# Performance work log

Hardware: AMD Instinct MI355X
Metric: run time of the kernel (lower is better)

## Reference

```python
import jax, jax.numpy as jnp
import numpy as np

N_NODES = 50000
N_FEAT = 128
N_EDGES = 800000
HEADS1 = 4
HID1 = 64
HID2 = 128
N_CLASSES = 10
N_GRAPHS = 512
NEG_SLOPE_ATT = 0.2   # GATConv attention leaky relu
NEG_SLOPE_ACT = 0.01  # F.leaky_relu default between layers


def setup_inputs() -> dict:
    key = jax.random.key(0)
    ks = jax.random.split(key, 20)
    s = 0.05
    inp = {
        'x': jax.random.normal(ks[0], (N_NODES, N_FEAT), dtype=jnp.float32),
        'edge_index': jax.random.randint(ks[1], (2, N_EDGES), 0, N_NODES, dtype=jnp.int64),
        'edge_attr': jax.random.normal(ks[2], (N_EDGES, 8), dtype=jnp.float32),
        'batch': jnp.sort(jax.random.randint(ks[3], (N_NODES,), 0, N_GRAPHS, dtype=jnp.int64)),
        # conv1: F -> HID1, heads=4, concat
        'W1': jax.random.normal(ks[4], (N_FEAT, HEADS1 * HID1), dtype=jnp.float32) * s,
        'a_src1': jax.random.normal(ks[5], (HEADS1, HID1), dtype=jnp.float32) * s,
        'a_dst1': jax.random.normal(ks[6], (HEADS1, HID1), dtype=jnp.float32) * s,
        'b1': jnp.zeros((HEADS1 * HID1,), dtype=jnp.float32),
        # conv2: 4*HID1 -> HID2, heads=1
        'W2': jax.random.normal(ks[7], (HEADS1 * HID1, HID2), dtype=jnp.float32) * s,
        'a_src2': jax.random.normal(ks[8], (1, HID2), dtype=jnp.float32) * s,
        'a_dst2': jax.random.normal(ks[9], (1, HID2), dtype=jnp.float32) * s,
        'b2': jnp.zeros((HID2,), dtype=jnp.float32),
        # conv3: HID2 -> N_CLASSES, heads=1
        'W3': jax.random.normal(ks[10], (HID2, N_CLASSES), dtype=jnp.float32) * s,
        'a_src3': jax.random.normal(ks[11], (1, N_CLASSES), dtype=jnp.float32) * s,
        'a_dst3': jax.random.normal(ks[12], (1, N_CLASSES), dtype=jnp.float32) * s,
        'b3': jnp.zeros((N_CLASSES,), dtype=jnp.float32),
    }
    return inp


def gat_conv(x, src, dst, W, a_src, a_dst, b, n_nodes, heads, ch):
    """PyG GATConv (concat=True, add_self_loops already applied in src/dst)."""
    h = (x @ W).reshape(n_nodes, heads, ch)            # [N,H,C]
    al_s = (h * a_src).sum(-1)                          # [N,H]
    al_d = (h * a_dst).sum(-1)                          # [N,H]
    e = jax.nn.leaky_relu(al_s[src] + al_d[dst], NEG_SLOPE_ATT)  # [E,H]
    # segment softmax over incoming edges per destination node
    m = jax.ops.segment_max(e, dst, num_segments=n_nodes)
    ex = jnp.exp(e - m[dst])
    den = jax.ops.segment_sum(ex, dst, num_segments=n_nodes)
    alpha = ex / (den[dst] + 1e-16)                     # [E,H]
    out = jax.ops.segment_sum(h[src] * alpha[..., None], dst, num_segments=n_nodes)
    return out.reshape(n_nodes, heads * ch) + b


def reference(x, edge_index, edge_attr, batch,
              W1, a_src1, a_dst1, b1,
              W2, a_src2, a_dst2, b2,
              W3, a_src3, a_dst3, b3):
    # GATConv adds self-loops by default; edge_attr unused (edge_dim=None)
    loops = jnp.arange(N_NODES, dtype=edge_index.dtype)
    src = jnp.concatenate([edge_index[0], loops])
    dst = jnp.concatenate([edge_index[1], loops])

    h = gat_conv(x, src, dst, W1, a_src1, a_dst1, b1, N_NODES, HEADS1, HID1)
    h = jax.nn.leaky_relu(h, NEG_SLOPE_ACT)
    h = gat_conv(h, src, dst, W2, a_src2, a_dst2, b2, N_NODES, 1, HID2)
    h = jax.nn.leaky_relu(h, NEG_SLOPE_ACT)
    h = gat_conv(h, src, dst, W3, a_src3, a_dst3, b3, N_NODES, 1, N_CLASSES)

    pooled = jax.ops.segment_sum(h, batch, num_segments=N_GRAPHS)  # global_add_pool
    return jax.nn.log_softmax(pooled, axis=1), pooled
```

## Files before the change

kernel.cpp:

```cpp
#include <hip/hip_runtime.h>
#include <math.h>

#define NNODES 50000
#define MPAD   50048
#define NFEAT  128
#define NEDGE  800000
#define ETOT   (NEDGE + NNODES)
#define H1     4
#define O1     256
#define C2     128
#define C3     10
#define NGRAPH 512

#define NBKT   196
#define NBLK1  831
#define EPB    1024
#define SCM    (NBKT * NBLK1)
#define SCB    637

typedef __attribute__((ext_vector_type(8))) short short8;
typedef __attribute__((ext_vector_type(4))) float f32x4;
typedef __attribute__((ext_vector_type(2))) float f32x2;

__device__ __forceinline__ unsigned short f2b(float f) {
  unsigned int u = __float_as_uint(f);
  u += 0x7fffu + ((u >> 16) & 1u);
  return (unsigned short)(u >> 16);
}
__device__ __forceinline__ float b2f(unsigned short u) {
  return __uint_as_float(((unsigned int)u) << 16);
}
__device__ __forceinline__ float readlane_f(float v, int l) {
  return __uint_as_float((unsigned)__builtin_amdgcn_readlane(__float_as_uint(v), l));
}


__global__ void k_prep(const float* __restrict__ W1, const float* __restrict__ as1,
                       const float* __restrict__ ad1,
                       float* __restrict__ was, float* __restrict__ wad) {
  int tid = threadIdx.x;
  int h = tid >> 7, k = tid & 127;
  float s = 0.f, d = 0.f;
  for (int j = 0; j < 64; ++j) {
    float w = W1[(size_t)k * 256 + h * 64 + j];
    s += w * as1[h * 64 + j];
    d += w * ad1[h * 64 + j];
  }
  was[h * 128 + k] = s;
  wad[h * 128 + k] = d;
}

#define NB_CVT 12500

__global__ __launch_bounds__(256) void k_front(
    const int* __restrict__ src_e, const int* __restrict__ dst_e,
    int* __restrict__ hists,
    const float* __restrict__ X, unsigned short* __restrict__ Xb,
    const float* __restrict__ W1,
    const float* __restrict__ was, const float* __restrict__ wad,
    float* __restrict__ als, float* __restrict__ ald,
    unsigned short* __restrict__ W1p,
    const float* __restrict__ W2, unsigned short* __restrict__ W2p,
    const float* __restrict__ W3, unsigned short* __restrict__ W3p) {
  const int b = blockIdx.x;
  const int tid = threadIdx.x;
  if (b < NBLK1) {
    __shared__ int h[NBKT];
    if (tid < NBKT) h[tid] = 0;
    __syncthreads();
    const int base = b * EPB;
#pragma unroll
    for (int r = 0; r < 4; ++r) {
      int e = base + r * 256 + tid;
      if (e < ETOT) {
        int d = (e < NEDGE) ? dst_e[e] : (e - NEDGE);
        atomicAdd(&h[d >> 8], 1);
      }
    }
    __syncthreads();
    if (tid < NBKT) hists[tid * NBLK1 + b] = h[tid];
  } else if (b < NBLK1 + NB_CVT) {
    const int n = (b - NBLK1) * 4 + (tid >> 6);
    const int lane = tid & 63;
    const int k0 = lane * 2;
    float2 xv = *(const float2*)(X + (size_t)n * 128 + k0);
    ushort2 o; o.x = f2b(xv.x); o.y = f2b(xv.y);
    *(ushort2*)(Xb + (size_t)n * 128 + k0) = o;
    float s[4], d[4];
#pragma unroll
    for (int h = 0; h < 4; ++h) {
      float2 wsv = *(const float2*)(was + h * 128 + k0);
      float2 wdv = *(const float2*)(wad + h * 128 + k0);
      s[h] = xv.x * wsv.x + xv.y * wsv.y;
      d[h] = xv.x * wdv.x + xv.y * wdv.y;
    }
#pragma unroll
    for (int m = 1; m < 64; m <<= 1)
#pragma unroll
      for (int h = 0; h < 4; ++h) { s[h] += __shfl_xor(s[h], m); d[h] += __shfl_xor(d[h], m); }
    if (lane == 0) {
#pragma unroll
      for (int h = 0; h < 4; ++h) {
        als[(size_t)n * 4 + h] = s[h];
        ald[(size_t)n * 4 + h] = d[h];
      }
    }
  } else if (b < NBLK1 + NB_CVT + 128) {
    int idx = (b - NBLK1 - NB_CVT) * 256 + tid;
    int h = idx >> 13, r = idx & 8191;
    int j = r & 7, lane = (r >> 3) & 63, t = r >> 9;
    int ks = t & 3, nt = t >> 2;
    int k = ks * 32 + (lane >> 4) * 8 + j;
    int n = nt * 16 + (lane & 15);
    W1p[idx] = f2b(W1[(size_t)k * 256 + h * 64 + n]);
  } else if (b < NBLK1 + NB_CVT + 256) {
    int idx = (b - NBLK1 - NB_CVT - 128) * 256 + tid;
    int j = idx & 7, lane = (idx >> 3) & 63, t = idx >> 9;
    int ks = t % 8, nt = t / 8;
    int k = ks * 32 + (lane >> 4) * 8 + j;
    int n = nt * 16 + (lane & 15);
    W2p[idx] = f2b(W2[(size_t)k * C2 + n]);
  } else {
    int idx = (b - NBLK1 - NB_CVT - 256) * 256 + tid;
    int j = idx & 7, lane = (idx >> 3) & 63, t = idx >> 9;
    int ks = t & 3, nt = t >> 2;
    int k = ks * 32 + (lane >> 4) * 8 + j;
    int n = nt * 16 + (lane & 15);
    W3p[idx] = f2b((n < C3) ? W3[(size_t)k * C3 + n] : 0.f);
  }
}


__global__ __launch_bounds__(256) void k_scanA2(const int* __restrict__ a,
                                                int* __restrict__ bsum) {
  int idx = blockIdx.x * 256 + threadIdx.x;
  int v = (idx < SCM) ? a[idx] : 0;
#pragma unroll
  for (int m = 1; m < 64; m <<= 1) v += __shfl_xor(v, m);
  __shared__ int ws[4];
  int lane = threadIdx.x & 63, wid = threadIdx.x >> 6;
  if (lane == 0) ws[wid] = v;
  __syncthreads();
  if (threadIdx.x == 0) bsum[blockIdx.x] = ws[0] + ws[1] + ws[2] + ws[3];
}

__global__ __launch_bounds__(256) void k_scanMid(int* __restrict__ bsum) {
  __shared__ int ws[4];
  __shared__ int carry_s;
  const int tid = threadIdx.x, lane = tid & 63, wid = tid >> 6;
  if (tid == 0) carry_s = 0;
  __syncthreads();
  for (int base = 0; base < SCB; base += 256) {
    int j = base + tid;
    int v = (j < SCB) ? bsum[j] : 0;
    int s = v;
#pragma unroll
    for (int m = 1; m < 64; m <<= 1) {
      int t = __shfl_up(s, m);
      if (lane >= m) s += t;
    }
    if (lane == 63) ws[wid] = s;
    __syncthreads();
    int woff = 0;
#pragma unroll
    for (int k = 0; k < 4; ++k)
      if (k < wid) woff += ws[k];
    int c = carry_s;
    int tot = ws[0] + ws[1] + ws[2] + ws[3];
    if (j < SCB) bsum[j] = c + woff + s - v;
    __syncthreads();
    if (tid == 0) carry_s = c + tot;
    __syncthreads();
  }
}

__global__ __launch_bounds__(256) void k_scanB2(int* __restrict__ a,
                                                const int* __restrict__ bsum,
                                                int* __restrict__ cb) {
  const int b = blockIdx.x, tid = threadIdx.x;
  const int lane = tid & 63, wid = tid >> 6;
  __shared__ int ws[4];
  int idx = b * 256 + tid;
  int v = (idx < SCM) ? a[idx] : 0;
  int s = v;
#pragma unroll
  for (int m = 1; m < 64; m <<= 1) {
    int t = __shfl_up(s, m);
    if (lane >= m) s += t;
  }
  if (lane == 63) ws[wid] = s;
  __syncthreads();
  int woff = 0;
#pragma unroll
  for (int k = 0; k < 4; ++k)
    if (k < wid) woff += ws[k];
  int excl = bsum[b] + woff + s - v;
  if (idx < SCM) {
    a[idx] = excl;
    if (idx % NBLK1 == 0) cb[idx / NBLK1] = excl;
  }
  if (b == 0 && tid == 0) cb[NBKT] = ETOT;
}


__global__ __launch_bounds__(256) void k_part1(const int* __restrict__ src_e,
                                               const int* __restrict__ dst_e,
                                               const int* __restrict__ offs,
                                               unsigned* __restrict__ coarse) {
  __shared__ int cur[NBKT];
  const int b = blockIdx.x;
  const int tid = threadIdx.x;
  if (tid < NBKT) cur[tid] = offs[tid * NBLK1 + b];
  __syncthreads();
  const int base = b * EPB;
#pragma unroll
  for (int r = 0; r < 4; ++r) {
    int e = base + r * 256 + tid;
    if (e < ETOT) {
      int d, s;
      if (e < NEDGE) { d = dst_e[e]; s = src_e[e]; }
      else           { d = e - NEDGE; s = e - NEDGE; }
      int pos = atomicAdd(&cur[d >> 8], 1);
      coarse[pos] = ((unsigned)d << 16) | (unsigned)s;
    }
  }
}


__global__ __launch_bounds__(256) void k_bucket(const unsigned* __restrict__ coarse,
                                                const int* __restrict__ cb,
                                                int* __restrict__ rowptr,
                                                int* __restrict__ srcs) {
  const int b = blockIdx.x;
  const int tid = threadIdx.x;
  const int lane = tid & 63, wid = tid >> 6;
  const int lo = cb[b], hi = cb[b + 1];
  __shared__ int h[256];
  __shared__ int cur[256];
  __shared__ int ws[4];
  h[tid] = 0;
  __syncthreads();
  for (int i = lo + tid; i < hi; i += 256)
    atomicAdd(&h[(coarse[i] >> 16) & 255], 1);
  __syncthreads();
  int v = h[tid];
  int s = v;
#pragma unroll
  for (int m = 1; m < 64; m <<= 1) {
    int t = __shfl_up(s, m);
    if (lane >= m) s += t;
  }
  if (lane == 63) ws[wid] = s;
  __syncthreads();
  int woff = 0;
#pragma unroll
  for (int k = 0; k < 4; ++k)
    if (k < wid) woff += ws[k];
  int ex = woff + s - v;
  cur[tid] = lo + ex;
  int d = b * 256 + tid;
  if (d < NNODES) rowptr[d] = lo + ex;
  if (b == NBKT - 1 && tid == 0) rowptr[NNODES] = ETOT;
  __syncthreads();
  for (int i = lo + tid; i < hi; i += 256) {
    unsigned c = coarse[i];
    int pos = atomicAdd(&cur[(c >> 16) & 255], 1);
    srcs[pos] = (int)(c & 0xffffu);
  }
}


__global__ __launch_bounds__(512) void k_aggP(const int* __restrict__ rowptr,
                                              const int* __restrict__ srcs,
                                              const unsigned short* __restrict__ Xb,
                                              const float* __restrict__ als,
                                              const float* __restrict__ ald,
                                              const unsigned short* __restrict__ W1p,
                                              const float* __restrict__ b1,
                                              unsigned short* __restrict__ act1) {
  __shared__ float exs[8][16][4];
  __shared__ unsigned short Pl[8][4][128];
  const int wv = threadIdx.x >> 6;
  const int n = blockIdx.x * 8 + wv;
  const int lane = threadIdx.x & 63;
  const int r0 = rowptr[n], r1 = rowptr[n + 1];
  const int e_lane = lane & 15, hh = lane >> 4;
  const float aldv = ald[(size_t)n * 4 + hh];
  const int ch0 = lane * 2;
  f32x2 ah0 = {0.f, 0.f}, ah1 = {0.f, 0.f}, ah2 = {0.f, 0.f}, ah3 = {0.f, 0.f};
  float den = 0.f;
  for (int i0 = r0; i0 < r1; i0 += 16) {
    const int take = r1 - i0;
    int sidx = srcs[min(i0 + e_lane, r1 - 1)];
    float ev = als[(size_t)sidx * 4 + hh] + aldv;
    ev = (ev > 0.f) ? ev : 0.2f * ev;
    float exv = (e_lane < take) ? __expf(ev) : 0.f;
    den += exv;
    exs[wv][e_lane][hh] = exv;
    unsigned hv[16];
#pragma unroll
    for (int m = 0; m < 16; ++m) {
      int s = __builtin_amdgcn_readlane(sidx, m);
      hv[m] = *(const unsigned*)(Xb + (size_t)s * 128 + ch0);
    }
#pragma unroll
    for (int m = 0; m < 16; ++m) {
      f32x2 e01 = *(const f32x2*)(&exs[wv][m][0]);
      f32x2 e23 = *(const f32x2*)(&exs[wv][m][2]);
      f32x2 x2;
      x2.x = __uint_as_float(hv[m] << 16);
      x2.y = __uint_as_float(hv[m] & 0xffff0000u);
      asm("v_pk_fma_f32 %0, %1, %2, %0 op_sel:[0,0,0] op_sel_hi:[1,0,1]"
          : "+v"(ah0) : "v"(x2), "v"(e01));
      asm("v_pk_fma_f32 %0, %1, %2, %0 op_sel:[0,1,0] op_sel_hi:[1,1,1]"
          : "+v"(ah1) : "v"(x2), "v"(e01));
      asm("v_pk_fma_f32 %0, %1, %2, %0 op_sel:[0,0,0] op_sel_hi:[1,0,1]"
          : "+v"(ah2) : "v"(x2), "v"(e23));
      asm("v_pk_fma_f32 %0, %1, %2, %0 op_sel:[0,1,0] op_sel_hi:[1,1,1]"
          : "+v"(ah3) : "v"(x2), "v"(e23));
    }
  }
#pragma unroll
  for (int m = 1; m < 16; m <<= 1) den += __shfl_xor(den, m);
  float acc[4][2] = {{ah0.x, ah0.y}, {ah1.x, ah1.y}, {ah2.x, ah2.y}, {ah3.x, ah3.y}};
#pragma unroll
  for (int h = 0; h < 4; ++h) {
    float rd = 1.f / (readlane_f(den, h * 16) + 1e-16f);
    ushort2 o; o.x = f2b(acc[h][0] * rd); o.y = f2b(acc[h][1] * rd);
    *(ushort2*)(&Pl[wv][h][ch0]) = o;
  }
  __syncthreads();

  const int row = lane & 15;
  const int k0 = (lane >> 4) * 8;
  const int col = lane & 15;
  const int rb = (lane >> 4) * 4;
#pragma unroll
  for (int u = 0; u < 2; ++u) {
    const int unit = wv + 8 * u;
    const int h = unit >> 2, nt = unit & 3;
    f32x4 acc2 = {};
#pragma unroll
    for (int ks = 0; ks < 4; ++ks) {
      short8 a{};
      if (row < 8) a = *(const short8*)(&Pl[row][h][ks * 32 + k0]);
      short8 b = *((const short8*)(W1p + (size_t)h * 8192) + nt * 256 + ks * 64 + lane);
      acc2 = __builtin_amdgcn_mfma_f32_16x16x32_bf16(a, b, acc2, 0, 0, 0);
    }
    const int ch = h * 64 + nt * 16 + col;
    const float bb = b1[ch];
#pragma unroll
    for (int j = 0; j < 4; ++j) {
      int r = rb + j;
      if (r < 8) {
        float v = acc2[j] + bb;
        v = (v > 0.f) ? v : 0.01f * v;
        act1[(size_t)(blockIdx.x * 8 + r) * 256 + ch] = f2b(v);
      }
    }
  }
}


template<int K, int N, int HEADS, int CREAL>
__global__ __launch_bounds__(256) void k_mm(const unsigned short* __restrict__ Xb,
                                            const unsigned short* __restrict__ Wp,
                                            unsigned short* __restrict__ Hout,
                                            const float* __restrict__ a_src,
                                            const float* __restrict__ a_dst,
                                            float* __restrict__ als,
                                            float* __restrict__ ald) {
  constexpr int KS = K / 32, NT = N / 16;
  constexpr int NTH = (NT + HEADS - 1) / HEADS;
  const int w = threadIdx.x >> 6, lane = threadIdx.x & 63;
  const int arow = blockIdx.x * 64 + w * 16 + (lane & 15);
  const int k0 = (lane >> 4) * 8;
  f32x4 acc[NT] = {};
  for (int ks = 0; ks < KS; ++ks) {
    short8 a = *(const short8*)(Xb + (size_t)arow * K + ks * 32 + k0);
    const short8* bp = (const short8*)Wp + (size_t)ks * 64 + lane;
#pragma unroll
    for (int nt = 0; nt < NT; ++nt) {
      short8 b = bp[(size_t)nt * KS * 64];
      acc[nt] = __builtin_amdgcn_mfma_f32_16x16x32_bf16(a, b, acc[nt], 0, 0, 0);
    }
  }
  const int col = lane & 15;
  const int rbase = blockIdx.x * 64 + w * 16 + (lane >> 4) * 4;
#pragma unroll
  for (int nt = 0; nt < NT; ++nt)
#pragma unroll
    for (int j = 0; j < 4; ++j)
      Hout[(size_t)(rbase + j) * N + nt * 16 + col] = f2b(acc[nt][j]);

  float av[NT], dv[NT];
#pragma unroll
  for (int nt = 0; nt < NT; ++nt) {
    int ch = nt * 16 + col;
    av[nt] = (ch < CREAL) ? a_src[ch] : 0.f;
    dv[nt] = (ch < CREAL) ? a_dst[ch] : 0.f;
  }
  float sa[HEADS][4], da[HEADS][4];
#pragma unroll
  for (int h = 0; h < HEADS; ++h)
#pragma unroll
    for (int j = 0; j < 4; ++j) { sa[h][j] = 0.f; da[h][j] = 0.f; }
#pragma unroll
  for (int nt = 0; nt < NT; ++nt) {
    int h = nt / NTH;
#pragma unroll
    for (int j = 0; j < 4; ++j) {
      sa[h][j] += acc[nt][j] * av[nt];
      da[h][j] += acc[nt][j] * dv[nt];
    }
  }
#pragma unroll
  for (int mask = 1; mask < 16; mask <<= 1)
#pragma unroll
    for (int h = 0; h < HEADS; ++h)
#pragma unroll
      for (int j = 0; j < 4; ++j) {
        sa[h][j] += __shfl_xor(sa[h][j], mask);
        da[h][j] += __shfl_xor(da[h][j], mask);
      }
  if (col == 0) {
#pragma unroll
    for (int j = 0; j < 4; ++j)
#pragma unroll
      for (int h = 0; h < HEADS; ++h) {
        als[(size_t)(rbase + j) * HEADS + h] = sa[h][j];
        ald[(size_t)(rbase + j) * HEADS + h] = da[h][j];
      }
  }
}


__global__ __launch_bounds__(512) void k_agg2(const int* __restrict__ rowptr,
                                              const int* __restrict__ srcs,
                                              const unsigned short* __restrict__ Hm,
                                              const float* __restrict__ als,
                                              const float* __restrict__ ald,
                                              const float* __restrict__ bias,
                                              const unsigned short* __restrict__ W3p,
                                              const float* __restrict__ as3,
                                              const float* __restrict__ ad3,
                                              unsigned short* __restrict__ H3b,
                                              float* __restrict__ als3,
                                              float* __restrict__ ald3) {
  __shared__ float exs2[8][16];
  __shared__ unsigned short Xl[8][128];
  const int wv = threadIdx.x >> 6;
  const int n = blockIdx.x * 8 + wv;
  const int lane = threadIdx.x & 63;
  const int r0 = rowptr[n], r1 = rowptr[n + 1];
  const int e_lane = lane & 15;
  const int ch0 = lane * 2;
  const float aldm = ald[n];
  f32x2 accP0 = {0.f, 0.f}, accP1 = {0.f, 0.f};
  float den = 0.f;
  for (int i0 = r0; i0 < r1; i0 += 16) {
    const int take = r1 - i0;
    int sidx = srcs[min(i0 + e_lane, r1 - 1)];
    float ev = als[sidx] + aldm;
    ev = (ev > 0.f) ? ev : 0.2f * ev;
    float exv = (lane < 16 && e_lane < take) ? __expf(ev) : 0.f;
    den += exv;
    if (lane < 16) exs2[wv][lane] = exv;
    unsigned hv[16];
#pragma unroll
    for (int m = 0; m < 16; ++m) {
      int s = __builtin_amdgcn_readlane(sidx, m);
      hv[m] = *(const unsigned*)(Hm + (size_t)s * C2 + ch0);
    }
#pragma unroll
    for (int m = 0; m < 16; m += 2) {
      f32x2 ep = *(const f32x2*)(&exs2[wv][m]);
      f32x2 xa, xb;
      xa.x = __uint_as_float(hv[m] << 16);
      xa.y = __uint_as_float(hv[m + 1] << 16);
      xb.x = __uint_as_float(hv[m] & 0xffff0000u);
      xb.y = __uint_as_float(hv[m + 1] & 0xffff0000u);
      asm("v_pk_fma_f32 %0, %1, %2, %0" : "+v"(accP0) : "v"(ep), "v"(xa));
      asm("v_pk_fma_f32 %0, %1, %2, %0" : "+v"(accP1) : "v"(ep), "v"(xb));
    }
  }
#pragma unroll
  for (int mask = 1; mask < 64; mask <<= 1) den += __shfl_xor(den, mask);
  float rden = 1.f / (den + 1e-16f);
  float v0 = (accP0.x + accP0.y) * rden + bias[ch0];
  float v1 = (accP1.x + accP1.y) * rden + bias[ch0 + 1];
  v0 = (v0 > 0.f) ? v0 : 0.01f * v0;
  v1 = (v1 > 0.f) ? v1 : 0.01f * v1;
  ushort2 o; o.x = f2b(v0); o.y = f2b(v1);
  *(ushort2*)(&Xl[wv][ch0]) = o;
  __syncthreads();

  if (wv == 0) {
    const int row = lane & 15;
    const int k0 = (lane >> 4) * 8;
    const int col = lane & 15;
    f32x4 acc2 = {};
#pragma unroll
    for (int ks = 0; ks < 4; ++ks) {
      short8 a{};
      if (row < 8) a = *(const short8*)(&Xl[row][ks * 32 + k0]);
      short8 b = *((const short8*)W3p + ks * 64 + lane);
      acc2 = __builtin_amdgcn_mfma_f32_16x16x32_bf16(a, b, acc2, 0, 0, 0);
    }
    const float av = (col < C3) ? as3[col] : 0.f;
    const float dv = (col < C3) ? ad3[col] : 0.f;
    const int rb = (lane >> 4) * 4;
#pragma unroll
    for (int j = 0; j < 4; ++j) {
      float hv = acc2[j];
      float sa = hv * av, da = hv * dv;
#pragma unroll
      for (int mask = 1; mask < 16; mask <<= 1) {
        sa += __shfl_xor(sa, mask);
        da += __shfl_xor(da, mask);
      }
      int r = rb + j;
      if (r < 8) {
        int node = blockIdx.x * 8 + r;
        H3b[(size_t)node * 16 + col] = f2b(hv);
        if (col == 0) { als3[node] = sa; ald3[node] = da; }
      }
    }
  }
}


__global__ __launch_bounds__(512) void k_agg3(const int* __restrict__ rowptr,
                                              const int* __restrict__ srcs,
                                              const unsigned short* __restrict__ Hm,
                                              const float* __restrict__ als,
                                              const float* __restrict__ ald,
                                              const float* __restrict__ bias,
                                              float* __restrict__ pooled,
                                              const int* __restrict__ batch) {
  __shared__ int   sid_s[8][4][16];
  __shared__ float exv_s[8][4][16];
  const int wv = threadIdx.x >> 6;
  const int lane = threadIdx.x & 63;
  const int g = lane >> 4, el = lane & 15;
  const int n = blockIdx.x * 32 + wv * 4 + g;
  const bool valid = n < NNODES;
  int r0 = 0, r1 = 0;
  float aldm = 0.f;
  if (valid) { r0 = rowptr[n]; r1 = rowptr[n + 1]; aldm = ald[n]; }
  float acc = 0.f, den = 0.f;
  for (int i0 = r0; i0 < r1; i0 += 16) {
    const int take = r1 - i0;
    int sidx = srcs[min(i0 + el, r1 - 1)];
    float ev = als[sidx] + aldm;
    ev = (ev > 0.f) ? ev : 0.2f * ev;
    float exv = (el < take) ? __expf(ev) : 0.f;
    den += exv;
    sid_s[wv][g][el] = sidx;
    exv_s[wv][g][el] = exv;
#pragma unroll
    for (int m = 0; m < 16; ++m) {
      int s = sid_s[wv][g][m];
      float ex = exv_s[wv][g][m];
      acc += ex * b2f(Hm[(size_t)s * 16 + el]);
    }
  }
#pragma unroll
  for (int mask = 1; mask < 16; mask <<= 1) den += __shfl_xor(den, mask);
  if (valid && el < C3) {
    float val = acc / (den + 1e-16f) + bias[el];
    atomicAdd(&pooled[(size_t)batch[n] * C3 + el], val);
  }
}


__global__ void k_lsm(const float* __restrict__ pooled, float* __restrict__ dout) {
  int g = blockIdx.x * 256 + threadIdx.x;
  if (g >= NGRAPH) return;
  float v[C3];
  float mx = -1e30f;
#pragma unroll
  for (int c = 0; c < C3; ++c) { v[c] = pooled[g * C3 + c]; mx = fmaxf(mx, v[c]); }
  float ssum = 0.f;
#pragma unroll
  for (int c = 0; c < C3; ++c) ssum += __expf(v[c] - mx);
  float lse = mx + __logf(ssum);
#pragma unroll
  for (int c = 0; c < C3; ++c) {
    dout[g * C3 + c] = v[c] - lse;
    dout[NGRAPH * C3 + g * C3 + c] = v[c];
  }
}


extern "C" void kernel_launch(void* const* d_in, const int* in_sizes, int n_in,
                              void* d_out, int out_size, void* d_ws, size_t ws_size,
                              hipStream_t stream) {
  (void)in_sizes; (void)n_in; (void)out_size; (void)ws_size;
  const float* x     = (const float*)d_in[0];
  const int*   eix   = (const int*)d_in[1];
  const int*   batch = (const int*)d_in[3];
  const float* W1 = (const float*)d_in[4];
  const float* as1 = (const float*)d_in[5];
  const float* ad1 = (const float*)d_in[6];
  const float* b1 = (const float*)d_in[7];
  const float* W2 = (const float*)d_in[8];
  const float* as2 = (const float*)d_in[9];
  const float* ad2 = (const float*)d_in[10];
  const float* b2 = (const float*)d_in[11];
  const float* W3 = (const float*)d_in[12];
  const float* as3 = (const float*)d_in[13];
  const float* ad3 = (const float*)d_in[14];
  const float* b3 = (const float*)d_in[15];
  const int* src_e = eix;
  const int* dst_e = eix + NEDGE;

  char* ws = (char*)d_ws;
  size_t off = 0;
  auto carve = [&](size_t bytes) -> char* {
    char* p = ws + off;
    off += (bytes + 511) & ~(size_t)511;
    return p;
  };
  int* hists  = (int*)carve((size_t)SCM * 4);
  int* bsum   = (int*)carve((size_t)SCB * 4);
  int* cb     = (int*)carve((size_t)(NBKT + 1) * 4);
  unsigned* coarse = (unsigned*)carve((size_t)ETOT * 4);
  int* rowptr = (int*)carve((size_t)(NNODES + 1) * 4);
  int* srcs   = (int*)carve((size_t)ETOT * 4);
  float* als  = (float*)carve((size_t)MPAD * H1 * 4);
  float* ald  = (float*)carve((size_t)MPAD * H1 * 4);
  float* als3 = (float*)carve((size_t)MPAD * 4);
  float* ald3 = (float*)carve((size_t)MPAD * 4);
  float* was  = (float*)carve((size_t)512 * 4);
  float* wad  = (float*)carve((size_t)512 * 4);
  unsigned short* Xb   = (unsigned short*)carve((size_t)MPAD * 128 * 2);
  unsigned short* act1 = (unsigned short*)carve((size_t)MPAD * 256 * 2);
  unsigned short* Hb   = (unsigned short*)carve((size_t)MPAD * 128 * 2);
  unsigned short* H3b  = (unsigned short*)carve((size_t)MPAD * 16 * 2);
  float* pooled = (float*)carve((size_t)NGRAPH * C3 * 4);
  unsigned short* W1p = (unsigned short*)carve((size_t)4 * 8192 * 2);
  unsigned short* W2p = (unsigned short*)carve((size_t)O1 * C2 * 2);
  unsigned short* W3p = (unsigned short*)carve((size_t)C2 * 16 * 2);

  hipMemsetAsync(pooled, 0, (size_t)NGRAPH * C3 * 4, stream);

  k_prep<<<1, 512, 0, stream>>>(W1, as1, ad1, was, wad);
  k_front<<<NBLK1 + NB_CVT + 264, 256, 0, stream>>>(
      src_e, dst_e, hists, x, Xb, W1, was, wad, als, ald, W1p, W2, W2p, W3, W3p);
  k_scanA2<<<SCB, 256, 0, stream>>>(hists, bsum);
  k_scanMid<<<1, 256, 0, stream>>>(bsum);
  k_scanB2<<<SCB, 256, 0, stream>>>(hists, bsum, cb);
  k_part1<<<NBLK1, 256, 0, stream>>>(src_e, dst_e, hists, coarse);
  k_bucket<<<NBKT, 256, 0, stream>>>(coarse, cb, rowptr, srcs);

  const int GB = MPAD / 64;
  const int NB8 = NNODES / 8;
  const int NB32 = (NNODES + 31) / 32;

  k_aggP<<<NB8, 512, 0, stream>>>(rowptr, srcs, Xb, als, ald, W1p, b1, act1);

  k_mm<O1, C2, 1, C2><<<GB, 256, 0, stream>>>(act1, W2p, Hb, as2, ad2, als, ald);
  k_agg2<<<NB8, 512, 0, stream>>>(rowptr, srcs, Hb, als, ald, b2,
                                  W3p, as3, ad3, H3b, als3, ald3);

  k_agg3<<<NB32, 512, 0, stream>>>(rowptr, srcs, H3b, als3, ald3, b3, pooled, batch);

  k_lsm<<<(NGRAPH + 255) / 256, 256, 0, stream>>>(pooled, (float*)d_out);
}
```

Before: 227.5 us.

## Move layer-1 projection out of aggregation into a fused W1+W2 GEMM kernel

The aggregation kernel now only computes the attention-weighted feature sums per head and writes them to a global buffer P. It no longer runs an in-block MFMA with half-empty 16-row tiles. A new kernel, k_mmX, applies the per-head W1 projection, bias and leaky ReLU on full 64-row tiles, keeps the activation in swizzled LDS, and immediately multiplies by W2 to produce H2 and its attention logits. This removes the act1 round trip through global memory and the block-wide sync in aggregation. In exchange it writes and reads the twice-as-large pre-projection buffer P.

```diff
diff --git a/kernel.cpp b/kernel.cpp
--- a/kernel.cpp
+++ b/kernel.cpp
@@ -275,11 +275,8 @@
                                               const unsigned short* __restrict__ Xb,
                                               const float* __restrict__ als,
                                               const float* __restrict__ ald,
-                                              const unsigned short* __restrict__ W1p,
-                                              const float* __restrict__ b1,
-                                              unsigned short* __restrict__ act1) {
+                                              unsigned short* __restrict__ P) {
   __shared__ float exs[8][16][4];
-  __shared__ unsigned short Pl[8][4][128];
   const int wv = threadIdx.x >> 6;
   const int n = blockIdx.x * 8 + wv;
   const int lane = threadIdx.x & 63;
@@ -327,110 +324,102 @@
   for (int h = 0; h < 4; ++h) {
     float rd = 1.f / (readlane_f(den, h * 16) + 1e-16f);
     ushort2 o; o.x = f2b(acc[h][0] * rd); o.y = f2b(acc[h][1] * rd);
-    *(ushort2*)(&Pl[wv][h][ch0]) = o;
-  }
-  __syncthreads();
-
-  const int row = lane & 15;
+    *(ushort2*)(P + ((size_t)n * 4 + h) * 128 + ch0) = o;
+  }
+}
+
+
+__global__ __launch_bounds__(256) void k_mmX(
+    const unsigned short* __restrict__ P,
+    const unsigned short* __restrict__ W1p, const float* __restrict__ b1,
+    const unsigned short* __restrict__ W2p,
+    const float* __restrict__ as2, const float* __restrict__ ad2,
+    unsigned short* __restrict__ Hout,
+    float* __restrict__ als, float* __restrict__ ald) {
+  __shared__ unsigned short actl[64 * 256];
+  const int wv = threadIdx.x >> 6, lane = threadIdx.x & 63;
+  const int row16 = lane & 15;
   const int k0 = (lane >> 4) * 8;
   const int col = lane & 15;
   const int rb = (lane >> 4) * 4;
-#pragma unroll
-  for (int u = 0; u < 2; ++u) {
-    const int unit = wv + 8 * u;
-    const int h = unit >> 2, nt = unit & 3;
-    f32x4 acc2 = {};
+
+  const int nodebase = blockIdx.x * 64 + wv * 16;
+#pragma unroll
+  for (int h = 0; h < 4; ++h) {
+    const unsigned short* Ph = P + ((size_t)(nodebase + row16) * 4 + h) * 128;
+    f32x4 acc[4] = {};
 #pragma unroll
     for (int ks = 0; ks < 4; ++ks) {
-      short8 a{};
-      if (row < 8) a = *(const short8*)(&Pl[row][h][ks * 32 + k0]);
-      short8 b = *((const short8*)(W1p + (size_t)h * 8192) + nt * 256 + ks * 64 + lane);
-      acc2 = __builtin_amdgcn_mfma_f32_16x16x32_bf16(a, b, acc2, 0, 0, 0);
-    }
-    const int ch = h * 64 + nt * 16 + col;
-    const float bb = b1[ch];
+      short8 a = *(const short8*)(Ph + ks * 32 + k0);
+      const short8* bp = (const short8*)(W1p + (size_t)h * 8192) + ks * 64 + lane;
+#pragma unroll
+      for (int nt = 0; nt < 4; ++nt) {
+        short8 b = bp[nt * 256];
+        acc[nt] = __builtin_amdgcn_mfma_f32_16x16x32_bf16(a, b, acc[nt], 0, 0, 0);
+      }
+    }
+#pragma unroll
+    for (int nt = 0; nt < 4; ++nt) {
+      int ch = h * 64 + nt * 16 + col;
+      float bb = b1[ch];
+#pragma unroll
+      for (int j = 0; j < 4; ++j) {
+        int row = wv * 16 + rb + j;
+        float v = acc[nt][j] + bb;
+        v = (v > 0.f) ? v : 0.01f * v;
+        unsigned byte = (unsigned)(row * 512 + ch * 2) ^ (unsigned)((row & 7) << 4);
+        *(unsigned short*)((char*)actl + byte) = f2b(v);
+      }
+    }
+  }
+  __syncthreads();
+
+  const int arow = wv * 16 + row16;
+  f32x4 acc2[8] = {};
+#pragma unroll
+  for (int ks = 0; ks < 8; ++ks) {
+    unsigned byte = (unsigned)(arow * 512 + (ks * 32 + k0) * 2) ^
+                    (unsigned)((arow & 7) << 4);
+    short8 a = *(const short8*)((const char*)actl + byte);
+    const short8* bp = (const short8*)W2p + ks * 64 + lane;
+#pragma unroll
+    for (int nt = 0; nt < 8; ++nt) {
+      short8 b = bp[(size_t)nt * 512];
+      acc2[nt] = __builtin_amdgcn_mfma_f32_16x16x32_bf16(a, b, acc2[nt], 0, 0, 0);
+    }
+  }
+  const int rbase = blockIdx.x * 64 + wv * 16 + rb;
+  float av[8], dv[8];
+#pragma unroll
+  for (int nt = 0; nt < 8; ++nt) {
+    int ch = nt * 16 + col;
+    av[nt] = as2[ch];
+    dv[nt] = ad2[ch];
+#pragma unroll
+    for (int j = 0; j < 4; ++j)
+      Hout[(size_t)(rbase + j) * C2 + ch] = f2b(acc2[nt][j]);
+  }
+  float sa[4] = {0.f, 0.f, 0.f, 0.f}, da[4] = {0.f, 0.f, 0.f, 0.f};
+#pragma unroll
+  for (int nt = 0; nt < 8; ++nt)
 #pragma unroll
     for (int j = 0; j < 4; ++j) {
-      int r = rb + j;
-      if (r < 8) {
-        float v = acc2[j] + bb;
-        v = (v > 0.f) ? v : 0.01f * v;
-        act1[(size_t)(blockIdx.x * 8 + r) * 256 + ch] = f2b(v);
-      }
-    }
-  }
-}
-
-
-template<int K, int N, int HEADS, int CREAL>
-__global__ __launch_bounds__(256) void k_mm(const unsigned short* __restrict__ Xb,
-                                            const unsigned short* __restrict__ Wp,
-                                            unsigned short* __restrict__ Hout,
-                                            const float* __restrict__ a_src,
-                                            const float* __restrict__ a_dst,
-                                            float* __restrict__ als,
-                                            float* __restrict__ ald) {
-  constexpr int KS = K / 32, NT = N / 16;
-  constexpr int NTH = (NT + HEADS - 1) / HEADS;
-  const int w = threadIdx.x >> 6, lane = threadIdx.x & 63;
-  const int arow = blockIdx.x * 64 + w * 16 + (lane & 15);
-  const int k0 = (lane >> 4) * 8;
-  f32x4 acc[NT] = {};
-  for (int ks = 0; ks < KS; ++ks) {
-    short8 a = *(const short8*)(Xb + (size_t)arow * K + ks * 32 + k0);
-    const short8* bp = (const short8*)Wp + (size_t)ks * 64 + lane;
-#pragma unroll
-    for (int nt = 0; nt < NT; ++nt) {
-      short8 b = bp[(size_t)nt * KS * 64];
-      acc[nt] = __builtin_amdgcn_mfma_f32_16x16x32_bf16(a, b, acc[nt], 0, 0, 0);
-    }
-  }
-  const int col = lane & 15;
-  const int rbase = blockIdx.x * 64 + w * 16 + (lane >> 4) * 4;
-#pragma unroll
-  for (int nt = 0; nt < NT; ++nt)
-#pragma unroll
-    for (int j = 0; j < 4; ++j)
-      Hout[(size_t)(rbase + j) * N + nt * 16 + col] = f2b(acc[nt][j]);
-
-  float av[NT], dv[NT];
-#pragma unroll
-  for (int nt = 0; nt < NT; ++nt) {
-    int ch = nt * 16 + col;
-    av[nt] = (ch < CREAL) ? a_src[ch] : 0.f;
-    dv[nt] = (ch < CREAL) ? a_dst[ch] : 0.f;
-  }
-  float sa[HEADS][4], da[HEADS][4];
-#pragma unroll
-  for (int h = 0; h < HEADS; ++h)
-#pragma unroll
-    for (int j = 0; j < 4; ++j) { sa[h][j] = 0.f; da[h][j] = 0.f; }
-#pragma unroll
-  for (int nt = 0; nt < NT; ++nt) {
-    int h = nt / NTH;
+      sa[j] += acc2[nt][j] * av[nt];
+      da[j] += acc2[nt][j] * dv[nt];
+    }
+#pragma unroll
+  for (int mask = 1; mask < 16; mask <<= 1)
 #pragma unroll
     for (int j = 0; j < 4; ++j) {
-      sa[h][j] += acc[nt][j] * av[nt];
-      da[h][j] += acc[nt][j] * dv[nt];
-    }
-  }
-#pragma unroll
-  for (int mask = 1; mask < 16; mask <<= 1)
-#pragma unroll
-    for (int h = 0; h < HEADS; ++h)
-#pragma unroll
-      for (int j = 0; j < 4; ++j) {
-        sa[h][j] += __shfl_xor(sa[h][j], mask);
-        da[h][j] += __shfl_xor(da[h][j], mask);
-      }
+      sa[j] += __shfl_xor(sa[j], mask);
+      da[j] += __shfl_xor(da[j], mask);
+    }
   if (col == 0) {
 #pragma unroll
-    for (int j = 0; j < 4; ++j)
-#pragma unroll
-      for (int h = 0; h < HEADS; ++h) {
-        als[(size_t)(rbase + j) * HEADS + h] = sa[h][j];
-        ald[(size_t)(rbase + j) * HEADS + h] = da[h][j];
-      }
+    for (int j = 0; j < 4; ++j) {
+      als[rbase + j] = sa[j];
+      ald[rbase + j] = da[j];
+    }
   }
 }
 
@@ -634,10 +623,10 @@
   float* ald3 = (float*)carve((size_t)MPAD * 4);
   float* was  = (float*)carve((size_t)512 * 4);
   float* wad  = (float*)carve((size_t)512 * 4);
-  unsigned short* Xb   = (unsigned short*)carve((size_t)MPAD * 128 * 2);
-  unsigned short* act1 = (unsigned short*)carve((size_t)MPAD * 256 * 2);
-  unsigned short* Hb   = (unsigned short*)carve((size_t)MPAD * 128 * 2);
-  unsigned short* H3b  = (unsigned short*)carve((size_t)MPAD * 16 * 2);
+  unsigned short* Xb  = (unsigned short*)carve((size_t)MPAD * 128 * 2);
+  unsigned short* P   = (unsigned short*)carve((size_t)MPAD * 512 * 2);
+  unsigned short* Hb  = (unsigned short*)carve((size_t)MPAD * 128 * 2);
+  unsigned short* H3b = (unsigned short*)carve((size_t)MPAD * 16 * 2);
   float* pooled = (float*)carve((size_t)NGRAPH * C3 * 4);
   unsigned short* W1p = (unsigned short*)carve((size_t)4 * 8192 * 2);
   unsigned short* W2p = (unsigned short*)carve((size_t)O1 * C2 * 2);
@@ -658,9 +647,9 @@
   const int NB8 = NNODES / 8;
   const int NB32 = (NNODES + 31) / 32;
 
-  k_aggP<<<NB8, 512, 0, stream>>>(rowptr, srcs, Xb, als, ald, W1p, b1, act1);
-
-  k_mm<O1, C2, 1, C2><<<GB, 256, 0, stream>>>(act1, W2p, Hb, as2, ad2, als, ald);
+  k_aggP<<<NB8, 512, 0, stream>>>(rowptr, srcs, Xb, als, ald, P);
+  k_mmX<<<GB, 256, 0, stream>>>(P, W1p, b1, W2p, as2, ad2, Hb, als, ald);
+
   k_agg2<<<NB8, 512, 0, stream>>>(rowptr, srcs, Hb, als, ald, b2,
                                   W3p, as3, ad3, H3b, als3, ald3);
 
```

Result: faster. 222.0 us (-2.4%).
